# Kernel optimization log

Hardware: AMD Instinct MI355X
Metric: run time of the kernel (lower is better)

Reference implementation:

```python
import jax, jax.numpy as jnp
import numpy as np
import math

D_MODEL = 512
D_HEAD = 64
N_HEADS = D_MODEL // D_HEAD  # 8
COND = 768
K = 7        # neighborhood kernel size
EPS = 1e-6


def _rope_freqs():
    # RoPE(dim=d_head//2, n_heads): freqs geometric in [pi, 10*pi), shape [n_heads, d_head//4]
    dim = D_HEAD // 2
    n = N_HEADS * dim // 2
    freqs = jnp.exp(jnp.linspace(math.log(math.pi), math.log(10.0 * math.pi), n + 1)[:-1])
    return freqs.reshape(dim // 2, N_HEADS).T  # [nh, d_head//4]


def _rms_norm(x, scale, eps):
    mean_sq = jnp.mean(x * x, axis=-1, keepdims=True)
    return x * (scale * jax.lax.rsqrt(mean_sq + eps))


def _apply_rotary(x, theta):
    # rotate first 2*d dims of head dim, leave the rest untouched
    d = theta.shape[-1]
    x1, x2, rest = x[..., :d], x[..., d:2 * d], x[..., 2 * d:]
    cos, sin = jnp.cos(theta), jnp.sin(theta)
    return jnp.concatenate([x1 * cos - x2 * sin, x2 * cos + x1 * sin, rest], axis=-1)


def _nb_idx(L, k):
    # NATTEN border handling: window shifts (clamps) so every query sees exactly k keys
    i = np.arange(L)
    start = np.clip(i - k // 2, 0, L - k)
    return jnp.asarray(start[:, None] + np.arange(k)[None, :])  # [L, k]


def setup_inputs() -> dict:
    key = jax.random.key(0)
    ks = jax.random.split(key, 7)
    N, H, W = 2, 32, 32
    x = jax.random.normal(ks[0], (N, H, W, D_MODEL), jnp.float32)
    pos = jax.random.uniform(ks[1], (N, H, W, 1), jnp.float32, -1.0, 1.0)
    cond = jax.random.normal(ks[2], (N, COND), jnp.float32)
    w_cond = jax.random.normal(ks[3], (D_MODEL, COND), jnp.float32) * 0.02
    w_qkv = jax.random.normal(ks[4], (3 * D_MODEL, D_MODEL), jnp.float32) * 0.02
    scale = jnp.full((N_HEADS,), 10.0, jnp.float32)
    w_out = jax.random.normal(ks[5], (D_MODEL, D_MODEL), jnp.float32) * 0.02
    return {"x": x, "pos": pos, "cond": cond, "w_cond": w_cond,
            "w_qkv": w_qkv, "scale": scale, "w_out": w_out}


def reference(x, pos, cond, w_cond, w_qkv, scale, w_out):
    N, H, W, C = x.shape
    skip = x
    # AdaRMSNorm: rms_norm(x, linear(cond) + 1)
    norm_scale = cond @ w_cond.T + 1.0                  # [N, C]
    xn = _rms_norm(x, norm_scale[:, None, None, :], EPS)
    # qkv projection -> [3, N, nh, H, W, e]
    qkv = (xn @ w_qkv.T).reshape(N, H, W, 3, N_HEADS, D_HEAD)
    qkv = qkv.transpose(3, 0, 4, 1, 2, 5)
    q, k, v = qkv[0], qkv[1], qkv[2]                    # [N, nh, H, W, e]
    # cosine-sim scaling
    sq = jnp.sqrt(scale)[:, None, None, None]           # [nh,1,1,1]
    q = q * (sq * jax.lax.rsqrt(jnp.sum(q * q, -1, keepdims=True) + 1e-6))
    k = k * (sq * jax.lax.rsqrt(jnp.sum(k * k, -1, keepdims=True) + 1e-6))
    # RoPE
    theta = pos[..., None, :] * _rope_freqs()           # [N,H,W,nh,e/4]
    theta = jnp.moveaxis(theta, -2, -4)                 # [N,nh,H,W,e/4]
    q = _apply_rotary(q, theta)
    k = _apply_rotary(k, theta)
    # 2D neighborhood attention (NATTEN, dilation 1)
    ih, iw = _nb_idx(H, K), _nb_idx(W, K)
    Knb = k[:, :, ih][:, :, :, :, iw]                   # [N,nh,H,K,W,K,e]
    Vnb = v[:, :, ih][:, :, :, :, iw]
    qk = jnp.einsum('ncije,nciajbe->ncijab', q, Knb)    # [N,nh,H,W,K,K]
    a = jax.nn.softmax(qk.reshape(N, N_HEADS, H, W, K * K), axis=-1)
    a = a.reshape(N, N_HEADS, H, W, K, K)
    o = jnp.einsum('ncijab,nciajbe->ncije', a, Vnb)     # [N,nh,H,W,e]
    o = o.transpose(0, 2, 3, 1, 4).reshape(N, H, W, C)
    return o @ w_out.T + skip
```

## Files before the change

kernel.cpp:

```cpp
#include <hip/hip_runtime.h>

typedef unsigned short u16;
typedef unsigned int u32;
typedef __bf16 bf16x8 __attribute__((ext_vector_type(8)));
typedef float f32x4 __attribute__((ext_vector_type(4)));

__device__ __forceinline__ float bf2f(u16 v) {
    union { u32 u; float f; } c; c.u = ((u32)v) << 16; return c.f;
}
__device__ __forceinline__ u16 f2bf(float f) {
    union { float f; u32 u; } c; c.f = f;
    u32 u = c.u + 0x7fffu + ((c.u >> 16) & 1u);
    return (u16)(u >> 16);
}

__global__ __launch_bounds__(256) void setup_kernel(
    const float* __restrict__ cond, const float* __restrict__ w_cond,
    const float* __restrict__ x, float* __restrict__ ns, float* __restrict__ inv)
{
    int lane = threadIdx.x & 63;
    int b = blockIdx.x;
    if (b < 256) {
        int wid = b * 4 + (threadIdx.x >> 6);
        int n = wid >> 9, c = wid & 511;
        const float* cp = cond + n * 768;
        const float* wp = w_cond + (size_t)c * 768;
        float s = 0.f;
        #pragma unroll
        for (int j = 0; j < 12; j++)
            s += cp[lane + j * 64] * wp[lane + j * 64];
        #pragma unroll
        for (int d = 1; d < 64; d <<= 1) s += __shfl_xor(s, d);
        if (lane == 0) ns[wid] = s + 1.f;
    } else {
        int p = (b - 256) * 4 + (threadIdx.x >> 6);
        const float* xp = x + (size_t)p * 512;
        float s = 0.f;
        #pragma unroll
        for (int j = 0; j < 8; j++) { float v = xp[lane + j * 64]; s += v * v; }
        #pragma unroll
        for (int d = 1; d < 64; d <<= 1) s += __shfl_xor(s, d);
        if (lane == 0) inv[p] = rsqrtf(s * (1.f / 512.f) + 1e-6f);
    }
}

__global__ __launch_bounds__(256) void convert_kernel(
    const float* __restrict__ x, const float* __restrict__ ns, const float* __restrict__ inv,
    const float* __restrict__ w_qkv, const float* __restrict__ w_out,
    u16* __restrict__ xn, u16* __restrict__ wqkvb, u16* __restrict__ woutb)
{
    int b = blockIdx.x;
    const float* src; u16* dst; size_t i4;
    bool rms = false;
    if (b < 1024)      { src = x;     dst = xn;    i4 = (size_t)(b)        * 1024 + threadIdx.x * 4; rms = true; }
    else if (b < 1792) { src = w_qkv; dst = wqkvb; i4 = (size_t)(b - 1024) * 1024 + threadIdx.x * 4; }
    else               { src = w_out; dst = woutb; i4 = (size_t)(b - 1792) * 1024 + threadIdx.x * 4; }
    float4 v = *(const float4*)(src + i4);
    if (rms) {
        int p = (int)(i4 >> 9), c = (int)(i4 & 511);
        float iv = inv[p];
        float4 nv = *(const float4*)(ns + (p >> 10) * 512 + c);
        v.x *= nv.x * iv; v.y *= nv.y * iv; v.z *= nv.z * iv; v.w *= nv.w * iv;
    }
    ushort4 o; o.x = f2bf(v.x); o.y = f2bf(v.y); o.z = f2bf(v.z); o.w = f2bf(v.w);
    *(ushort4*)(dst + i4) = o;
}

template<bool OUT_BF16, bool ADD_SKIP>
__global__ __launch_bounds__(256) void gemm_bt(
    const u16* __restrict__ A, const u16* __restrict__ B,
    float* __restrict__ Cf, u16* __restrict__ Cb, const float* __restrict__ skip,
    int N, int K)
{
    __shared__ __align__(16) u16 As[64][40];
    __shared__ __align__(16) u16 Bs[64][40];
    int tid = threadIdx.x;
    int lane = tid & 63;
    int w = tid >> 6;
    int wm = w >> 1, wn = w & 1;
    int bm = blockIdx.x * 64, bn = blockIdx.y * 64;
    int lrow = tid >> 2, lc8 = (tid & 3) * 8;

    f32x4 zero = {0.f, 0.f, 0.f, 0.f};
    f32x4 acc[2][2];
    acc[0][0] = zero; acc[0][1] = zero; acc[1][0] = zero; acc[1][1] = zero;

    const u16* Ap = A + (size_t)(bm + lrow) * K + lc8;
    const u16* Bp = B + (size_t)(bn + lrow) * K + lc8;
    int r = lane & 15, kq = (lane >> 4) * 8;

    for (int k0 = 0; k0 < K; k0 += 32) {
        *(uint4*)&As[lrow][lc8] = *(const uint4*)(Ap + k0);
        *(uint4*)&Bs[lrow][lc8] = *(const uint4*)(Bp + k0);
        __syncthreads();
        #pragma unroll
        for (int ri = 0; ri < 2; ri++) {
            bf16x8 af = *(const bf16x8*)&As[wm * 32 + ri * 16 + r][kq];
            #pragma unroll
            for (int ci = 0; ci < 2; ci++) {
                bf16x8 bfr = *(const bf16x8*)&Bs[wn * 32 + ci * 16 + r][kq];
                acc[ri][ci] = __builtin_amdgcn_mfma_f32_16x16x32_bf16(af, bfr, acc[ri][ci], 0, 0, 0);
            }
        }
        __syncthreads();
    }

    #pragma unroll
    for (int ri = 0; ri < 2; ri++)
    #pragma unroll
    for (int ci = 0; ci < 2; ci++) {
        int col = bn + wn * 32 + ci * 16 + (lane & 15);
        int row0 = bm + wm * 32 + ri * 16 + (lane >> 4) * 4;
        #pragma unroll
        for (int reg = 0; reg < 4; reg++) {
            size_t idx = (size_t)(row0 + reg) * N + col;
            float v = acc[ri][ci][reg];
            if (ADD_SKIP) v += skip[idx];
            if (OUT_BF16) Cb[idx] = f2bf(v);
            else Cf[idx] = v;
        }
    }
}

__global__ __launch_bounds__(256) void rope_plane_kernel(
    const u16* __restrict__ qkvb, const float* __restrict__ pos, const float* __restrict__ scale,
    u16* __restrict__ qp, u16* __restrict__ kp, u16* __restrict__ vp)
{
    int lane = threadIdx.x & 63;
    int wid = blockIdx.x * 4 + (threadIdx.x >> 6);
    int qk = wid >> 14;
    int rem = wid & 16383;
    int h = rem & 7, p = rem >> 3;
    float v = bf2f(qkvb[(size_t)p * 1536 + qk * 512 + h * 64 + lane]);
    float res = v;
    if (qk < 2) {
        float ss = v * v;
        #pragma unroll
        for (int d = 1; d < 64; d <<= 1) ss += __shfl_xor(ss, d);
        float sc = sqrtf(scale[h]) * rsqrtf(ss + 1e-6f);
        v *= sc;
        float partner = __shfl_xor(v, 16);
        res = v;
        if (lane < 32) {
            int t = lane & 15;
            float fr = 3.14159265358979323846f * expf((float)(t * 8 + h) * (2.302585092994046f / 128.f));
            float th = pos[p] * fr;
            float cs = cosf(th), sn = sinf(th);
            res = (lane < 16) ? (v * cs - partner * sn) : (v * cs + partner * sn);
        }
    }
    u16* plane = (qk == 0) ? qp : (qk == 1) ? kp : vp;
    size_t dst = ((size_t)((p >> 10) * 8 + h) * 1024 + (p & 1023)) * 64 + lane;
    plane[dst] = f2bf(res);
}

__global__ __launch_bounds__(256) void attn_kernel(
    const u16* __restrict__ qp, const u16* __restrict__ kp, const u16* __restrict__ vp,
    u16* __restrict__ o)
{
    __shared__ u32 klu[4][49 * 33];
    __shared__ float qls[4][64];
    int w = threadIdx.x >> 6, lane = threadIdx.x & 63;
    int wid = blockIdx.x * 4 + w;
    int h = wid & 7, p = wid >> 3;
    int n = p >> 10, i = (p >> 5) & 31, j = p & 31;
    int si = min(max(i - 3, 0), 25), sj = min(max(j - 3, 0), 25);

    size_t base = (size_t)(n * 8 + h) * 1024 * 64;
    qls[w][lane] = bf2f(qp[base + (size_t)(p & 1023) * 64 + lane]);
    u16* kls = (u16*)klu[w];
    {
        const u16* kb = kp + base + (size_t)(si * 32 + sj) * 64 + lane;
        #pragma unroll
        for (int a = 0; a < 49; a++)
            kls[a * 66 + lane] = kb[((a / 7) * 32 + (a % 7)) * 64];
    }
    __syncthreads();

    float score = -1e30f;
    if (lane < 49) {
        float s = 0.f;
        const u32* kr = &klu[w][lane * 33];
        const float* qr = qls[w];
        #pragma unroll
        for (int e2 = 0; e2 < 32; e2++) {
            u32 v = kr[e2];
            s += qr[2 * e2] * bf2f((u16)(v & 0xffff))
               + qr[2 * e2 + 1] * bf2f((u16)(v >> 16));
        }
        score = s;
    }
    float m = score;
    #pragma unroll
    for (int d = 1; d < 64; d <<= 1) m = fmaxf(m, __shfl_xor(m, d));
    float ex = (lane < 49) ? expf(score - m) : 0.f;
    float s = ex;
    #pragma unroll
    for (int d = 1; d < 64; d <<= 1) s += __shfl_xor(s, d);
    float pr = ex * __frcp_rn(s);

    float acc = 0.f;
    {
        const u16* vb = vp + base + (size_t)(si * 32 + sj) * 64 + lane;
        #pragma unroll
        for (int a = 0; a < 49; a++)
            acc += __shfl(pr, a) * bf2f(vb[((a / 7) * 32 + (a % 7)) * 64]);
    }
    o[(size_t)p * 512 + h * 64 + lane] = f2bf(acc);
}

extern "C" void kernel_launch(void* const* d_in, const int* in_sizes, int n_in,
                              void* d_out, int out_size, void* d_ws, size_t ws_size,
                              hipStream_t stream)
{
    const float *x = nullptr, *pos = nullptr, *cond = nullptr, *w_cond = nullptr,
                *w_qkv = nullptr, *scale = nullptr, *w_out = nullptr;
    for (int i = 0; i < n_in; i++) {
        switch (in_sizes[i]) {
            case 1048576: x      = (const float*)d_in[i]; break;
            case 2048:    pos    = (const float*)d_in[i]; break;
            case 1536:    cond   = (const float*)d_in[i]; break;
            case 393216:  w_cond = (const float*)d_in[i]; break;
            case 786432:  w_qkv  = (const float*)d_in[i]; break;
            case 8:       scale  = (const float*)d_in[i]; break;
            case 262144:  w_out  = (const float*)d_in[i]; break;
            default: break;
        }
    }
    float* out = (float*)d_out;

    char* ws = (char*)d_ws;
    float* ns    = (float*)ws;
    float* inv   = (float*)(ws + 4096);
    u16*   qkvb  = (u16*)(ws + 12288);
    u16*   xn    = (u16*)(ws + 12288 + 6291456);
    u16*   wqkvb = (u16*)(ws + 12288 + 8388608);
    u16*   woutb = (u16*)(ws + 12288 + 9961472);
    u16*   qp    = (u16*)(ws + 12288 + 10485760);
    u16*   kp    = (u16*)(ws + 12288 + 12582912);
    u16*   vp    = (u16*)(ws + 12288 + 14680064);
    u16*   ob    = (u16*)(ws + 12288 + 16777216);

    setup_kernel<<<768, 256, 0, stream>>>(cond, w_cond, x, ns, inv);
    convert_kernel<<<2048, 256, 0, stream>>>(x, ns, inv, w_qkv, w_out, xn, wqkvb, woutb);
    gemm_bt<true, false><<<dim3(32, 24), 256, 0, stream>>>(xn, wqkvb, nullptr, qkvb, nullptr, 1536, 512);
    rope_plane_kernel<<<12288, 256, 0, stream>>>(qkvb, pos, scale, qp, kp, vp);
    attn_kernel<<<4096, 256, 0, stream>>>(qp, kp, vp, ob);
    gemm_bt<false, true><<<dim3(32, 8), 256, 0, stream>>>(ob, woutb, out, nullptr, x, 512, 512);
}
```

Baseline: 128.2 us.

## Tile neighborhood attention per 8x8 query block using MFMA for QK and PV

Replaces the one-wave-per-query scalar attention kernel with a block-tiled kernel. Each block handles an 8x8 query tile for one head and loads the shared 14x14 key/value halo into LDS once. QK^T and PV are computed densely with bf16 MFMA over all 196 halo keys, and out-of-window keys are masked before the softmax. This trades redundant global K/V loads and scalar FMAs for extra masked MFMA work, fp16 score storage and a transposed V layout in LDS.

New measurement: 121.1 us. 1.06x faster.

```diff
diff --git a/kernel.cpp b/kernel.cpp
--- a/kernel.cpp
+++ b/kernel.cpp
@@ -154,59 +154,134 @@
     plane[dst] = f2bf(res);
 }
 
-__global__ __launch_bounds__(256) void attn_kernel(
+__global__ __launch_bounds__(256) void attn_mfma(
     const u16* __restrict__ qp, const u16* __restrict__ kp, const u16* __restrict__ vp,
-    u16* __restrict__ o)
-{
-    __shared__ u32 klu[4][49 * 33];
-    __shared__ float qls[4][64];
-    int w = threadIdx.x >> 6, lane = threadIdx.x & 63;
-    int wid = blockIdx.x * 4 + w;
-    int h = wid & 7, p = wid >> 3;
-    int n = p >> 10, i = (p >> 5) & 31, j = p & 31;
-    int si = min(max(i - 3, 0), 25), sj = min(max(j - 3, 0), 25);
-
-    size_t base = (size_t)(n * 8 + h) * 1024 * 64;
-    qls[w][lane] = bf2f(qp[base + (size_t)(p & 1023) * 64 + lane]);
-    u16* kls = (u16*)klu[w];
+    u16* __restrict__ ob)
+{
+    __shared__ __align__(16) u16 Kb[208 * 72];
+    __shared__ __align__(16) u16 Sb[64 * 232];
+
+    int tid = threadIdx.x, lane = tid & 63, w = tid >> 6;
+    int bx = blockIdx.x;
+    int n = bx >> 7, h = (bx >> 4) & 7, t = bx & 15;
+    int ti = (t >> 2) * 8, tj = (t & 3) * 8;
+    int r0 = min(max(ti - 3, 0), 18), c0 = min(max(tj - 3, 0), 18);
+    const u16* qpl = qp + ((size_t)(n * 8 + h) << 16);
+    const u16* kpl = kp + ((size_t)(n * 8 + h) << 16);
+    const u16* vpl = vp + ((size_t)(n * 8 + h) << 16);
+
+    for (int g = tid; g < 1568; g += 256) {
+        int nb = g >> 3, k8 = (g & 7) << 3;
+        int ar = nb / 14, ac = nb - ar * 14;
+        *(uint4*)&Kb[nb * 72 + k8] =
+            *(const uint4*)&kpl[(size_t)((r0 + ar) * 32 + c0 + ac) * 64 + k8];
+    }
+    __syncthreads();
+
+    int m = lane & 15, quad = lane >> 4;
     {
-        const u16* kb = kp + base + (size_t)(si * 32 + sj) * 64 + lane;
-        #pragma unroll
-        for (int a = 0; a < 49; a++)
-            kls[a * 66 + lane] = kb[((a / 7) * 32 + (a % 7)) * 64];
+        int r = w * 16 + m;
+        int tok = (ti + (r >> 3)) * 32 + (tj + (r & 7));
+        bf16x8 qf0 = *(const bf16x8*)&qpl[(size_t)tok * 64 + quad * 8];
+        bf16x8 qf1 = *(const bf16x8*)&qpl[(size_t)tok * 64 + 32 + quad * 8];
+        _Float16* sp = (_Float16*)Sb;
+        #pragma unroll
+        for (int nt = 0; nt < 13; nt++) {
+            f32x4 acc = {0.f, 0.f, 0.f, 0.f};
+            bf16x8 b0 = *(const bf16x8*)&Kb[(nt * 16 + m) * 72 + quad * 8];
+            bf16x8 b1 = *(const bf16x8*)&Kb[(nt * 16 + m) * 72 + 32 + quad * 8];
+            acc = __builtin_amdgcn_mfma_f32_16x16x32_bf16(qf0, b0, acc, 0, 0, 0);
+            acc = __builtin_amdgcn_mfma_f32_16x16x32_bf16(qf1, b1, acc, 0, 0, 0);
+            #pragma unroll
+            for (int reg = 0; reg < 4; reg++)
+                sp[(w * 16 + quad * 4 + reg) * 232 + nt * 16 + m] = (_Float16)acc[reg];
+        }
     }
     __syncthreads();
 
-    float score = -1e30f;
-    if (lane < 49) {
-        float s = 0.f;
-        const u32* kr = &klu[w][lane * 33];
-        const float* qr = qls[w];
-        #pragma unroll
-        for (int e2 = 0; e2 < 32; e2++) {
-            u32 v = kr[e2];
-            s += qr[2 * e2] * bf2f((u16)(v & 0xffff))
-               + qr[2 * e2 + 1] * bf2f((u16)(v >> 16));
-        }
-        score = s;
-    }
-    float m = score;
-    #pragma unroll
-    for (int d = 1; d < 64; d <<= 1) m = fmaxf(m, __shfl_xor(m, d));
-    float ex = (lane < 49) ? expf(score - m) : 0.f;
-    float s = ex;
-    #pragma unroll
-    for (int d = 1; d < 64; d <<= 1) s += __shfl_xor(s, d);
-    float pr = ex * __frcp_rn(s);
-
-    float acc = 0.f;
+    for (int g = tid; g < 1568; g += 256) {
+        int nb = g >> 3, k8 = (g & 7) << 3;
+        int ar = nb / 14, ac = nb - ar * 14;
+        uint4 v4 = *(const uint4*)&vpl[(size_t)((r0 + ar) * 32 + c0 + ac) * 64 + k8];
+        u32 uu[4] = {v4.x, v4.y, v4.z, v4.w};
+        #pragma unroll
+        for (int e = 0; e < 4; e++) {
+            Kb[(k8 + 2 * e) * 234 + nb]     = (u16)(uu[e] & 0xffff);
+            Kb[(k8 + 2 * e + 1) * 234 + nb] = (u16)(uu[e] >> 16);
+        }
+    }
+    for (int g = tid; g < 1792; g += 256) {
+        int d = g / 28, nb = 196 + (g - d * 28);
+        Kb[d * 234 + nb] = 0;
+    }
+
     {
-        const u16* vb = vp + base + (size_t)(si * 32 + sj) * 64 + lane;
-        #pragma unroll
-        for (int a = 0; a < 49; a++)
-            acc += __shfl(pr, a) * bf2f(vb[((a / 7) * 32 + (a % 7)) * 64]);
-    }
-    o[(size_t)p * 512 + h * 64 + lane] = f2bf(acc);
+        int l16 = lane & 15, g4 = lane >> 4;
+        #pragma unroll
+        for (int it = 0; it < 4; it++) {
+            int rr = w * 16 + it * 4 + g4;
+            int i2 = ti + (rr >> 3), j2 = tj + (rr & 7);
+            int alo = min(max(i2 - 3, 0), 25) - r0;
+            int blo = min(max(j2 - 3, 0), 25) - c0;
+            const _Float16* sp = (const _Float16*)&Sb[rr * 232];
+            float vals[14];
+            float mx = -1e30f;
+            #pragma unroll
+            for (int c = 0; c < 14; c++) {
+                int col = l16 + c * 16;
+                float v = -1e30f;
+                if (col < 196) {
+                    int ar = col / 14, ac = col - ar * 14;
+                    if (ar >= alo && ar < alo + 7 && ac >= blo && ac < blo + 7)
+                        v = (float)sp[col];
+                }
+                vals[c] = v; mx = fmaxf(mx, v);
+            }
+            #pragma unroll
+            for (int d = 1; d < 16; d <<= 1) mx = fmaxf(mx, __shfl_xor(mx, d));
+            float s = 0.f;
+            #pragma unroll
+            for (int c = 0; c < 14; c++) {
+                float e = (vals[c] > -1e29f) ? expf(vals[c] - mx) : 0.f;
+                vals[c] = e; s += e;
+            }
+            #pragma unroll
+            for (int d = 1; d < 16; d <<= 1) s += __shfl_xor(s, d);
+            float rs = __frcp_rn(s);
+            u16* pp = &Sb[rr * 232];
+            #pragma unroll
+            for (int c = 0; c < 14; c++)
+                pp[l16 + c * 16] = f2bf(vals[c] * rs);
+        }
+    }
+    __syncthreads();
+
+    f32x4 oacc[4];
+    #pragma unroll
+    for (int nt = 0; nt < 4; nt++) { f32x4 z = {0.f,0.f,0.f,0.f}; oacc[nt] = z; }
+    #pragma unroll
+    for (int ks = 0; ks < 7; ks++) {
+        bf16x8 pa = *(const bf16x8*)&Sb[(w * 16 + m) * 232 + ks * 32 + quad * 8];
+        #pragma unroll
+        for (int nt = 0; nt < 4; nt++) {
+            int ad = (nt * 16 + m) * 234 + ks * 32 + quad * 8;
+            union { u32 u[4]; bf16x8 v; } vb;
+            vb.u[0] = *(const u32*)&Kb[ad];
+            vb.u[1] = *(const u32*)&Kb[ad + 2];
+            vb.u[2] = *(const u32*)&Kb[ad + 4];
+            vb.u[3] = *(const u32*)&Kb[ad + 6];
+            oacc[nt] = __builtin_amdgcn_mfma_f32_16x16x32_bf16(pa, vb.v, oacc[nt], 0, 0, 0);
+        }
+    }
+    #pragma unroll
+    for (int nt = 0; nt < 4; nt++) {
+        #pragma unroll
+        for (int reg = 0; reg < 4; reg++) {
+            int rr = w * 16 + quad * 4 + reg;
+            int tok = (ti + (rr >> 3)) * 32 + (tj + (rr & 7));
+            ob[(size_t)(n * 1024 + tok) * 512 + h * 64 + nt * 16 + m] = f2bf(oacc[nt][reg]);
+        }
+    }
 }
 
 extern "C" void kernel_launch(void* const* d_in, const int* in_sizes, int n_in,
@@ -245,6 +320,6 @@
     convert_kernel<<<2048, 256, 0, stream>>>(x, ns, inv, w_qkv, w_out, xn, wqkvb, woutb);
     gemm_bt<true, false><<<dim3(32, 24), 256, 0, stream>>>(xn, wqkvb, nullptr, qkvb, nullptr, 1536, 512);
     rope_plane_kernel<<<12288, 256, 0, stream>>>(qkvb, pos, scale, qp, kp, vp);
-    attn_kernel<<<4096, 256, 0, stream>>>(qp, kp, vp, ob);
+    attn_mfma<<<256, 256, 0, stream>>>(qp, kp, vp, ob);
     gemm_bt<false, true><<<dim3(32, 8), 256, 0, stream>>>(ob, woutb, out, nullptr, x, 512, 512);
 }
```
